# Optimization experiments

Hardware: AMD Instinct MI355X
Metric: run time of the kernel (lower is better)

## Reference

```python
import jax, jax.numpy as jnp
import numpy as np
import math

B, SQ, SK, DQ, DK, DV = 8, 1024, 1024, 512, 512, 512


def setup_inputs() -> dict:
    key = jax.random.key(0)
    ks = jax.random.split(key, 12)
    s = lambda fan_in: 1.0 / math.sqrt(fan_in)
    return {
        "Q": jax.random.normal(ks[0], (B, SQ, DQ), jnp.float32),
        "K": jax.random.normal(ks[1], (B, SK, DK), jnp.float32),
        "Wq": jax.random.uniform(ks[2], (DV, DQ), jnp.float32, -s(DQ), s(DQ)),
        "bq": jax.random.uniform(ks[3], (DV,), jnp.float32, -s(DQ), s(DQ)),
        "Wk": jax.random.uniform(ks[4], (DV, DK), jnp.float32, -s(DK), s(DK)),
        "bk": jax.random.uniform(ks[5], (DV,), jnp.float32, -s(DK), s(DK)),
        "Wv": jax.random.uniform(ks[6], (DV, DK), jnp.float32, -s(DK), s(DK)),
        "bv": jax.random.uniform(ks[7], (DV,), jnp.float32, -s(DK), s(DK)),
        "Wo": jax.random.uniform(ks[8], (DV, DV), jnp.float32, -s(DV), s(DV)),
        "bo": jax.random.uniform(ks[9], (DV,), jnp.float32, -s(DV), s(DV)),
        "num_heads": 8,
    }


def reference(Q, K, Wq, bq, Wk, bk, Wv, bv, Wo, bo, num_heads):
    dim_V = Wq.shape[0]
    dh = dim_V // num_heads
    b, sq, _ = Q.shape
    sk = K.shape[1]
    # projections (torch Linear: x @ W.T + b)
    Qp = Q @ Wq.T + bq                      # [B, Sq, Dv]
    Kp = K @ Wk.T + bk                      # [B, Sk, Dv]
    Vp = K @ Wv.T + bv                      # [B, Sk, Dv]
    # manual head split (split along feature, cat along batch) == reshape to heads
    Qh = Qp.reshape(b, sq, num_heads, dh)   # [B, Sq, H, dh]
    Kh = Kp.reshape(b, sk, num_heads, dh)
    Vh = Vp.reshape(b, sk, num_heads, dh)
    # NOTE: scale is sqrt(dim_V), not sqrt(head_dim), as in the source.
    scores = jnp.einsum("bqhd,bkhd->bhqk", Qh, Kh) / jnp.sqrt(
        jnp.asarray(dim_V, Qh.dtype))
    A = jax.nn.softmax(scores, axis=-1)     # [B, H, Sq, Sk]
    ctx = jnp.einsum("bhqk,bkhd->bqhd", A, Vh)
    O = (Qh + ctx).reshape(b, sq, dim_V)    # residual on projected Q, merge heads
    O = O + jax.nn.relu(O @ Wo.T + bo)      # FFN residual
    return O
```

## Files before the change

### kernel.cpp

```cpp
#include <hip/hip_runtime.h>

typedef unsigned short u16;
typedef __attribute__((ext_vector_type(8))) short short8;
typedef __attribute__((ext_vector_type(4))) float f32x4;
typedef __attribute__((ext_vector_type(2))) unsigned uint2v;

__device__ __forceinline__ u16 f2bf(float f) {
  union { float f; unsigned u; } v; v.f = f;
  unsigned r = v.u + 0x7FFFu + ((v.u >> 16) & 1u);
  return (u16)(r >> 16);
}
__device__ __forceinline__ float bf2f(u16 u) {
  union { unsigned u; float f; } v; v.u = ((unsigned)u) << 16;
  return v.f;
}
__device__ __forceinline__ void gload_lds16(const u16* g, u16* l) {
  __builtin_amdgcn_global_load_lds((const __attribute__((address_space(1))) void*)g,
                                   (__attribute__((address_space(3))) void*)l,
                                   16, 0, 0);
}

#if __has_builtin(__builtin_amdgcn_exp2f)
#define EXP2(x) __builtin_amdgcn_exp2f(x)
#else
#define EXP2(x) exp2f(x)
#endif

#define BATCH 8
#define SEQ   1024
#define DIM   512
#define NH    8
#define DH    64
#define MROWS (BATCH * SEQ)

__global__ void cvt_all(const float* __restrict__ Q, const float* __restrict__ K,
                        const float* __restrict__ Wq, const float* __restrict__ Wk,
                        const float* __restrict__ Wv, const float* __restrict__ Wo,
                        u16* __restrict__ Qbf, u16* __restrict__ Kbf,
                        u16* __restrict__ Wbf) {
  const int gb = blockIdx.x;
  const float4* src;
  u16* dst;
  int i;
  if (gb < 4096) {
    src = (const float4*)Q; dst = Qbf; i = gb * 256 + threadIdx.x;
  } else if (gb < 8192) {
    src = (const float4*)K; dst = Kbf; i = (gb - 4096) * 256 + threadIdx.x;
  } else {
    const int wb = gb - 8192;
    const int wsel = wb >> 8;
    const float* w = (wsel == 0) ? Wq : (wsel == 1) ? Wk : (wsel == 2) ? Wv : Wo;
    src = (const float4*)w;
    dst = Wbf + (size_t)wsel * (DIM * DIM);
    i = (wb & 255) * 256 + threadIdx.x;
  }
  float4 v = src[i];
  ushort4 r;
  r.x = f2bf(v.x); r.y = f2bf(v.y); r.z = f2bf(v.z); r.w = f2bf(v.w);
  *(ushort4*)&dst[i * 4] = r;
}

__device__ __forceinline__ void gemm_core(const u16* __restrict__ A,
                                          const u16* __restrict__ W,
                                          u16* ldsA, u16* ldsB,
                                          int tid, int m0, int n0,
                                          f32x4 acc[4][4]) {
  const int lane = tid & 63;
  const int wv = tid >> 6;
  const int wr = wv >> 1, wc = wv & 1;
  const int lr = lane & 15, lg = lane >> 4;
  const int wbase = tid & 192;

#define STAGE(buf, kt)                                                          \
  {                                                                             \
    _Pragma("unroll")                                                           \
    for (int i = 0; i < 2; ++i) {                                               \
      const int T = i * 256 + tid;                                              \
      const int row = T & 127, kc = T >> 7;                                     \
      const int koff = (kt) * 32 + kc * 8;                                      \
      gload_lds16(A + (size_t)(m0 + row) * DIM + koff,                          \
                  ldsA + (buf) * 4096 + (i * 256 + wbase) * 8);                 \
      gload_lds16(W + (size_t)(n0 + row) * DIM + koff,                          \
                  ldsB + (buf) * 4096 + (i * 256 + wbase) * 8);                 \
    }                                                                           \
  }

  STAGE(0, 0);
  __syncthreads();
  int cur = 0;
#pragma unroll 1
  for (int kt = 0; kt < 16; ++kt) {
    if (kt < 15) STAGE(cur ^ 1, kt + 1);
    short8 av[4], bw[4];
#pragma unroll
    for (int m = 0; m < 4; ++m)
      av[m] = *(const short8*)(ldsA + cur * 4096 + (lg * 128 + wr * 64 + m * 16 + lr) * 8);
#pragma unroll
    for (int n = 0; n < 4; ++n)
      bw[n] = *(const short8*)(ldsB + cur * 4096 + (lg * 128 + wc * 64 + n * 16 + lr) * 8);
#pragma unroll
    for (int m = 0; m < 4; ++m)
#pragma unroll
      for (int n = 0; n < 4; ++n)
        acc[m][n] = __builtin_amdgcn_mfma_f32_16x16x32_bf16(av[m], bw[n], acc[m][n], 0, 0, 0);
    __syncthreads();
    cur ^= 1;
  }
#undef STAGE
}

__global__ __launch_bounds__(256, 2) void proj_gemm(
    const u16* __restrict__ Qbf, const u16* __restrict__ Kbf,
    const u16* __restrict__ Wbf,
    const float* __restrict__ bq, const float* __restrict__ bk,
    const float* __restrict__ bv,
    u16* __restrict__ Qp, u16* __restrict__ Kp, u16* __restrict__ VpT) {
  __shared__ alignas(16) u16 ldsA[2 * 4096];
  __shared__ alignas(16) u16 ldsB[2 * 4096];

  const int tid = threadIdx.x;
  const int z = blockIdx.z;
  const int m0 = blockIdx.x * 128;
  const int n0 = blockIdx.y * 128;

  const u16* A = (z == 0) ? Qbf : Kbf;
  const u16* W = Wbf + (size_t)z * (DIM * DIM);
  const float* bias = (z == 0) ? bq : (z == 1) ? bk : bv;

  f32x4 acc[4][4] = {};
  gemm_core(A, W, ldsA, ldsB, tid, m0, n0, acc);

  const int lane = tid & 63;
  const int wv = tid >> 6;
  const int wr = wv >> 1, wc = wv & 1;
  const int lr = lane & 15, lg = lane >> 4;

  float bn[4];
#pragma unroll
  for (int n = 0; n < 4; ++n) bn[n] = bias[n0 + wc * 64 + n * 16 + lr];

  if (z < 2) {
    u16* outp = (z == 0) ? Qp : Kp;
#pragma unroll
    for (int m = 0; m < 4; ++m)
#pragma unroll
      for (int n = 0; n < 4; ++n)
#pragma unroll
        for (int r = 0; r < 4; ++r) {
          const int row = m0 + wr * 64 + m * 16 + lg * 4 + r;
          const int col = n0 + wc * 64 + n * 16 + lr;
          outp[(size_t)row * DIM + col] = f2bf(acc[m][n][r] + bn[n]);
        }
  } else {
#pragma unroll
    for (int m = 0; m < 4; ++m)
#pragma unroll
      for (int n = 0; n < 4; ++n) {
        const int grow = m0 + wr * 64 + m * 16 + lg * 4;
        const int b = grow >> 10;
        const int s = grow & 1023;
        const int col = n0 + wc * 64 + n * 16 + lr;
        ushort4 pk;
        pk.x = f2bf(acc[m][n][0] + bn[n]);
        pk.y = f2bf(acc[m][n][1] + bn[n]);
        pk.z = f2bf(acc[m][n][2] + bn[n]);
        pk.w = f2bf(acc[m][n][3] + bn[n]);
        *(ushort4*)&VpT[(size_t)b * (DIM * SEQ) + (size_t)col * SEQ + s] = pk;
      }
  }
}

__global__ __launch_bounds__(512, 4) void attn_kernel(
    const u16* __restrict__ Qp, const u16* __restrict__ Kp,
    const u16* __restrict__ VpT, u16* __restrict__ Opre) {
  __shared__ alignas(16) u16 klds[2][8192];
  __shared__ alignas(16) u16 vlds[2][8192];
  __shared__ alignas(16) u16 plds[8][64 * 16];

  const int tid = threadIdx.x;
  const int lane = tid & 63, wv = tid >> 6;
  const int lr = lane & 15, lg = lane >> 4;
  const int q0 = blockIdx.y * 128;
  const int b = blockIdx.x >> 3, h = blockIdx.x & 7;
  const size_t rowbase = (size_t)b * SEQ;
  const int hoff = h * DH;

  const float csc = 0.063762f;
  short8 aq[2];
#pragma unroll
  for (int t = 0; t < 2; ++t) {
    short8 raw = *(const short8*)(Qp + (rowbase + q0 + wv * 16 + lr) * DIM +
                                  hoff + t * 32 + lg * 8);
    short8 s;
#pragma unroll
    for (int j = 0; j < 8; ++j) s[j] = (short)f2bf(bf2f((u16)raw[j]) * csc);
    aq[t] = s;
  }

#define STAGEKV(buf, kt)                                                        \
  {                                                                             \
    const int ks0_ = (kt) * 128;                                                \
    _Pragma("unroll")                                                           \
    for (int i = 0; i < 2; ++i) {                                               \
      const int T = i * 512 + tid;                                              \
      const int krr = T & 127, kcc = T >> 7;                                    \
      gload_lds16(Kp + (rowbase + ks0_ + krr) * DIM + hoff + kcc * 8,           \
                  &klds[buf][(i * 512 + (tid & 448)) * 8]);                     \
      const int vrr = T & 63, vcc = T >> 6;                                     \
      gload_lds16(VpT + (size_t)b * (DIM * SEQ) + (size_t)(hoff + vrr) * SEQ +  \
                      ks0_ + vcc * 8,                                           \
                  &vlds[buf][(i * 512 + (tid & 448)) * 8]);                     \
    }                                                                           \
  }

  u16* pw = &plds[wv][0];
  unsigned pbase = (unsigned)(uintptr_t)(__attribute__((address_space(3))) u16*)pw;
  const unsigned ta00 = pbase + (unsigned)lg * 128u;
  const unsigned ta01 = ta00 + 128u;
  const unsigned ta10 = ta00 + 1024u;
  const unsigned ta11 = ta00 + 1152u;

  float l_r[4] = {0.f, 0.f, 0.f, 0.f};
  f32x4 o_acc[4] = {};

  STAGEKV(0, 0);
  __syncthreads();

  int cur = 0;
#pragma unroll 1
  for (int kt = 0; kt < 8; ++kt) {
    if (kt < 7) STAGEKV(cur ^ 1, kt + 1);

#pragma unroll
    for (int hh = 0; hh < 2; ++hh) {
      f32x4 sa[4] = {};
      __builtin_amdgcn_s_setprio(1);
#pragma unroll
      for (int t = 0; t < 2; ++t)
#pragma unroll
        for (int f = 0; f < 4; ++f) {
          short8 bk_ = *(const short8*)(
              &klds[cur][((lg + 4 * t) * 128 + hh * 64 + f * 16 + lr) * 8]);
          sa[f] = __builtin_amdgcn_mfma_f32_16x16x32_bf16(aq[t], bk_, sa[f], 0, 0, 0);
        }
      __builtin_amdgcn_s_setprio(0);

      short8 bvf[8];
#pragma unroll
      for (int n = 0; n < 4; ++n)
#pragma unroll
        for (int t = 0; t < 2; ++t)
          bvf[n * 2 + t] = *(const short8*)(
              &vlds[cur][((8 * hh + 4 * t + lg) * 64 + n * 16 + lr) * 8]);

#pragma unroll
      for (int f = 0; f < 4; ++f) {
        float p0 = EXP2(sa[f][0]);
        float p1 = EXP2(sa[f][1]);
        float p2 = EXP2(sa[f][2]);
        float p3 = EXP2(sa[f][3]);
        l_r[0] += p0; l_r[1] += p1; l_r[2] += p2; l_r[3] += p3;
        unsigned lo, hi;
        asm("v_cvt_pk_bf16_f32 %0, %1, %2" : "=v"(lo) : "v"(p0), "v"(p1));
        asm("v_cvt_pk_bf16_f32 %0, %1, %2" : "=v"(hi) : "v"(p2), "v"(p3));
        uint2v pk; pk.x = lo; pk.y = hi;
        *(uint2v*)&pw[(f * 16 + lr) * 16 + lg * 4] = pk;
      }

      asm volatile("s_waitcnt lgkmcnt(0)" ::: "memory");
      uint2v t00, t01, t10, t11;
      asm volatile("ds_read_b64_tr_b16 %0, %1" : "=v"(t00) : "v"(ta00));
      asm volatile("ds_read_b64_tr_b16 %0, %1" : "=v"(t01) : "v"(ta01));
      asm volatile("ds_read_b64_tr_b16 %0, %1" : "=v"(t10) : "v"(ta10));
      asm volatile("ds_read_b64_tr_b16 %0, %1" : "=v"(t11) : "v"(ta11));
      asm volatile("s_waitcnt lgkmcnt(0)" ::: "memory");
      __builtin_amdgcn_sched_barrier(0);

      short8 ap[2];
      {
        union { unsigned u[4]; short8 s; } u0, u1;
        u0.u[0] = t00.x; u0.u[1] = t00.y; u0.u[2] = t01.x; u0.u[3] = t01.y;
        u1.u[0] = t10.x; u1.u[1] = t10.y; u1.u[2] = t11.x; u1.u[3] = t11.y;
        ap[0] = u0.s; ap[1] = u1.s;
      }

      __builtin_amdgcn_s_setprio(1);
#pragma unroll
      for (int n = 0; n < 4; ++n)
#pragma unroll
        for (int t = 0; t < 2; ++t)
          o_acc[n] = __builtin_amdgcn_mfma_f32_16x16x32_bf16(ap[t], bvf[n * 2 + t], o_acc[n], 0, 0, 0);
      __builtin_amdgcn_s_setprio(0);
    }

    __syncthreads();
    cur ^= 1;
  }
#undef STAGEKV

  float inv[4];
#pragma unroll
  for (int r = 0; r < 4; ++r) {
    float v = l_r[r];
#pragma unroll
    for (int msk = 1; msk < 16; msk <<= 1) v += __shfl_xor(v, msk);
    inv[r] = 1.0f / v;
  }
#pragma unroll
  for (int n = 0; n < 4; ++n)
#pragma unroll
    for (int r = 0; r < 4; ++r) {
      const size_t row = rowbase + q0 + wv * 16 + lg * 4 + r;
      const int col = hoff + n * 16 + lr;
      const float ctx = o_acc[n][r] * inv[r];
      const float qv = bf2f(Qp[row * DIM + col]);
      Opre[row * DIM + col] = f2bf(qv + ctx);
    }
}

__global__ __launch_bounds__(256, 2) void ffn_gemm(
    const u16* __restrict__ Opre, const u16* __restrict__ Wo_bf,
    const float* __restrict__ bo, float* __restrict__ out) {
  __shared__ alignas(16) u16 ldsA[2 * 4096];
  __shared__ alignas(16) u16 ldsB[2 * 4096];

  const int tid = threadIdx.x;
  const int m0 = blockIdx.x * 128;
  const int n0 = blockIdx.y * 128;

  f32x4 acc[4][4] = {};
  gemm_core(Opre, Wo_bf, ldsA, ldsB, tid, m0, n0, acc);

  const int lane = tid & 63;
  const int wv = tid >> 6;
  const int wr = wv >> 1, wc = wv & 1;
  const int lr = lane & 15, lg = lane >> 4;

  float bn[4];
#pragma unroll
  for (int n = 0; n < 4; ++n) bn[n] = bo[n0 + wc * 64 + n * 16 + lr];

#pragma unroll
  for (int m = 0; m < 4; ++m)
#pragma unroll
    for (int n = 0; n < 4; ++n)
#pragma unroll
      for (int r = 0; r < 4; ++r) {
        const int row = m0 + wr * 64 + m * 16 + lg * 4 + r;
        const int col = n0 + wc * 64 + n * 16 + lr;
        const float v = acc[m][n][r] + bn[n];
        const float o = bf2f(Opre[(size_t)row * DIM + col]);
        out[(size_t)row * DIM + col] = o + fmaxf(v, 0.f);
      }
}

extern "C" void kernel_launch(void* const* d_in, const int* in_sizes, int n_in,
                              void* d_out, int out_size, void* d_ws, size_t ws_size,
                              hipStream_t stream) {
  const float* Q  = (const float*)d_in[0];
  const float* K  = (const float*)d_in[1];
  const float* Wq = (const float*)d_in[2];
  const float* bq = (const float*)d_in[3];
  const float* Wk = (const float*)d_in[4];
  const float* bk = (const float*)d_in[5];
  const float* Wv = (const float*)d_in[6];
  const float* bv = (const float*)d_in[7];
  const float* Wo = (const float*)d_in[8];
  const float* bo = (const float*)d_in[9];

  char* ws = (char*)d_ws;
  const size_t SZ = (size_t)MROWS * DIM * sizeof(u16);
  u16* Qbf  = (u16*)(ws + 0);
  u16* Kbf  = (u16*)(ws + SZ);
  u16* Wbf  = (u16*)(ws + 2 * SZ);
  u16* Qp   = (u16*)(ws + 2 * SZ + 4 * (size_t)(DIM * DIM) * sizeof(u16));
  u16* Kp   = (u16*)((char*)Qp + SZ);
  u16* VpT  = (u16*)((char*)Kp + SZ);
  u16* Opre = (u16*)(ws + 0);

  cvt_all<<<dim3(9216), 256, 0, stream>>>(Q, K, Wq, Wk, Wv, Wo, Qbf, Kbf, Wbf);
  proj_gemm<<<dim3(64, 4, 3), 256, 0, stream>>>(Qbf, Kbf, Wbf, bq, bk, bv, Qp, Kp, VpT);
  attn_kernel<<<dim3(64, 8), 512, 0, stream>>>(Qp, Kp, VpT, Opre);
  ffn_gemm<<<dim3(64, 4), 256, 0, stream>>>(Opre, Wbf + 3 * (DIM * DIM), bo, (float*)d_out);
}
```

Baseline: 98.53 us.

## Halve attention KV tile and compute softmax row sums with MFMA against ones

The attention kernel now stages 64-key K/V tiles instead of 128, which halves LDS use per block and doubles the number of loop iterations and __syncthreads barriers. The softmax denominator is no longer accumulated in fp32 with a cross-lane shuffle reduction at the end. Instead it comes from two extra MFMAs that multiply the bf16 P tile by a vector of ones. The smaller LDS footprint may allow more resident blocks, at the cost of more barriers, and the row sums now use bf16-rounded probabilities.

```diff
diff --git a/kernel.cpp b/kernel.cpp
--- a/kernel.cpp
+++ b/kernel.cpp
@@ -173,8 +173,8 @@
 __global__ __launch_bounds__(512, 4) void attn_kernel(
     const u16* __restrict__ Qp, const u16* __restrict__ Kp,
     const u16* __restrict__ VpT, u16* __restrict__ Opre) {
-  __shared__ alignas(16) u16 klds[2][8192];
-  __shared__ alignas(16) u16 vlds[2][8192];
+  __shared__ alignas(16) u16 klds[2][4096];
+  __shared__ alignas(16) u16 vlds[2][4096];
   __shared__ alignas(16) u16 plds[8][64 * 16];
 
   const int tid = threadIdx.x;
@@ -197,20 +197,19 @@
     aq[t] = s;
   }
 
+  short8 ones;
+#pragma unroll
+  for (int j = 0; j < 8; ++j) ones[j] = (short)0x3F80;
+
 #define STAGEKV(buf, kt)                                                        \
   {                                                                             \
-    const int ks0_ = (kt) * 128;                                                \
-    _Pragma("unroll")                                                           \
-    for (int i = 0; i < 2; ++i) {                                               \
-      const int T = i * 512 + tid;                                              \
-      const int krr = T & 127, kcc = T >> 7;                                    \
-      gload_lds16(Kp + (rowbase + ks0_ + krr) * DIM + hoff + kcc * 8,           \
-                  &klds[buf][(i * 512 + (tid & 448)) * 8]);                     \
-      const int vrr = T & 63, vcc = T >> 6;                                     \
-      gload_lds16(VpT + (size_t)b * (DIM * SEQ) + (size_t)(hoff + vrr) * SEQ +  \
-                      ks0_ + vcc * 8,                                           \
-                  &vlds[buf][(i * 512 + (tid & 448)) * 8]);                     \
-    }                                                                           \
+    const int ks0_ = (kt) * 64;                                                 \
+    const int rr = tid & 63, cc = tid >> 6;                                     \
+    gload_lds16(Kp + (rowbase + ks0_ + rr) * DIM + hoff + cc * 8,               \
+                &klds[buf][tid * 8]);                                           \
+    gload_lds16(VpT + (size_t)b * (DIM * SEQ) + (size_t)(hoff + rr) * SEQ +     \
+                    ks0_ + cc * 8,                                              \
+                &vlds[buf][tid * 8]);                                           \
   }
 
   u16* pw = &plds[wv][0];
@@ -220,7 +219,7 @@
   const unsigned ta10 = ta00 + 1024u;
   const unsigned ta11 = ta00 + 1152u;
 
-  float l_r[4] = {0.f, 0.f, 0.f, 0.f};
+  f32x4 l_acc = {};
   f32x4 o_acc[4] = {};
 
   STAGEKV(0, 0);
@@ -228,70 +227,66 @@
 
   int cur = 0;
 #pragma unroll 1
-  for (int kt = 0; kt < 8; ++kt) {
-    if (kt < 7) STAGEKV(cur ^ 1, kt + 1);
-
-#pragma unroll
-    for (int hh = 0; hh < 2; ++hh) {
-      f32x4 sa[4] = {};
-      __builtin_amdgcn_s_setprio(1);
+  for (int kt = 0; kt < 16; ++kt) {
+    if (kt < 15) STAGEKV(cur ^ 1, kt + 1);
+
+    f32x4 sa[4] = {};
+    __builtin_amdgcn_s_setprio(1);
+#pragma unroll
+    for (int t = 0; t < 2; ++t)
+#pragma unroll
+      for (int f = 0; f < 4; ++f) {
+        short8 bk_ = *(const short8*)(&klds[cur][((lg + 4 * t) * 64 + f * 16 + lr) * 8]);
+        sa[f] = __builtin_amdgcn_mfma_f32_16x16x32_bf16(aq[t], bk_, sa[f], 0, 0, 0);
+      }
+    __builtin_amdgcn_s_setprio(0);
+
+    short8 bvf[8];
+#pragma unroll
+    for (int n = 0; n < 4; ++n)
 #pragma unroll
       for (int t = 0; t < 2; ++t)
-#pragma unroll
-        for (int f = 0; f < 4; ++f) {
-          short8 bk_ = *(const short8*)(
-              &klds[cur][((lg + 4 * t) * 128 + hh * 64 + f * 16 + lr) * 8]);
-          sa[f] = __builtin_amdgcn_mfma_f32_16x16x32_bf16(aq[t], bk_, sa[f], 0, 0, 0);
-        }
-      __builtin_amdgcn_s_setprio(0);
-
-      short8 bvf[8];
-#pragma unroll
-      for (int n = 0; n < 4; ++n)
-#pragma unroll
-        for (int t = 0; t < 2; ++t)
-          bvf[n * 2 + t] = *(const short8*)(
-              &vlds[cur][((8 * hh + 4 * t + lg) * 64 + n * 16 + lr) * 8]);
-
-#pragma unroll
-      for (int f = 0; f < 4; ++f) {
-        float p0 = EXP2(sa[f][0]);
-        float p1 = EXP2(sa[f][1]);
-        float p2 = EXP2(sa[f][2]);
-        float p3 = EXP2(sa[f][3]);
-        l_r[0] += p0; l_r[1] += p1; l_r[2] += p2; l_r[3] += p3;
-        unsigned lo, hi;
-        asm("v_cvt_pk_bf16_f32 %0, %1, %2" : "=v"(lo) : "v"(p0), "v"(p1));
-        asm("v_cvt_pk_bf16_f32 %0, %1, %2" : "=v"(hi) : "v"(p2), "v"(p3));
-        uint2v pk; pk.x = lo; pk.y = hi;
-        *(uint2v*)&pw[(f * 16 + lr) * 16 + lg * 4] = pk;
-      }
-
-      asm volatile("s_waitcnt lgkmcnt(0)" ::: "memory");
-      uint2v t00, t01, t10, t11;
-      asm volatile("ds_read_b64_tr_b16 %0, %1" : "=v"(t00) : "v"(ta00));
-      asm volatile("ds_read_b64_tr_b16 %0, %1" : "=v"(t01) : "v"(ta01));
-      asm volatile("ds_read_b64_tr_b16 %0, %1" : "=v"(t10) : "v"(ta10));
-      asm volatile("ds_read_b64_tr_b16 %0, %1" : "=v"(t11) : "v"(ta11));
-      asm volatile("s_waitcnt lgkmcnt(0)" ::: "memory");
-      __builtin_amdgcn_sched_barrier(0);
-
-      short8 ap[2];
-      {
-        union { unsigned u[4]; short8 s; } u0, u1;
-        u0.u[0] = t00.x; u0.u[1] = t00.y; u0.u[2] = t01.x; u0.u[3] = t01.y;
-        u1.u[0] = t10.x; u1.u[1] = t10.y; u1.u[2] = t11.x; u1.u[3] = t11.y;
-        ap[0] = u0.s; ap[1] = u1.s;
-      }
-
-      __builtin_amdgcn_s_setprio(1);
-#pragma unroll
-      for (int n = 0; n < 4; ++n)
-#pragma unroll
-        for (int t = 0; t < 2; ++t)
-          o_acc[n] = __builtin_amdgcn_mfma_f32_16x16x32_bf16(ap[t], bvf[n * 2 + t], o_acc[n], 0, 0, 0);
-      __builtin_amdgcn_s_setprio(0);
+        bvf[n * 2 + t] = *(const short8*)(&vlds[cur][((lg + 4 * t) * 64 + n * 16 + lr) * 8]);
+
+#pragma unroll
+    for (int f = 0; f < 4; ++f) {
+      float p0 = EXP2(sa[f][0]);
+      float p1 = EXP2(sa[f][1]);
+      float p2 = EXP2(sa[f][2]);
+      float p3 = EXP2(sa[f][3]);
+      unsigned lo, hi;
+      asm("v_cvt_pk_bf16_f32 %0, %1, %2" : "=v"(lo) : "v"(p0), "v"(p1));
+      asm("v_cvt_pk_bf16_f32 %0, %1, %2" : "=v"(hi) : "v"(p2), "v"(p3));
+      uint2v pk; pk.x = lo; pk.y = hi;
+      *(uint2v*)&pw[(f * 16 + lr) * 16 + lg * 4] = pk;
     }
+
+    asm volatile("s_waitcnt lgkmcnt(0)" ::: "memory");
+    uint2v t00, t01, t10, t11;
+    asm volatile("ds_read_b64_tr_b16 %0, %1" : "=v"(t00) : "v"(ta00));
+    asm volatile("ds_read_b64_tr_b16 %0, %1" : "=v"(t01) : "v"(ta01));
+    asm volatile("ds_read_b64_tr_b16 %0, %1" : "=v"(t10) : "v"(ta10));
+    asm volatile("ds_read_b64_tr_b16 %0, %1" : "=v"(t11) : "v"(ta11));
+    asm volatile("s_waitcnt lgkmcnt(0)" ::: "memory");
+    __builtin_amdgcn_sched_barrier(0);
+
+    short8 ap[2];
+    {
+      union { unsigned u[4]; short8 s; } u0, u1;
+      u0.u[0] = t00.x; u0.u[1] = t00.y; u0.u[2] = t01.x; u0.u[3] = t01.y;
+      u1.u[0] = t10.x; u1.u[1] = t10.y; u1.u[2] = t11.x; u1.u[3] = t11.y;
+      ap[0] = u0.s; ap[1] = u1.s;
+    }
+
+    __builtin_amdgcn_s_setprio(1);
+#pragma unroll
+    for (int n = 0; n < 4; ++n)
+#pragma unroll
+      for (int t = 0; t < 2; ++t)
+        o_acc[n] = __builtin_amdgcn_mfma_f32_16x16x32_bf16(ap[t], bvf[n * 2 + t], o_acc[n], 0, 0, 0);
+    l_acc = __builtin_amdgcn_mfma_f32_16x16x32_bf16(ap[0], ones, l_acc, 0, 0, 0);
+    l_acc = __builtin_amdgcn_mfma_f32_16x16x32_bf16(ap[1], ones, l_acc, 0, 0, 0);
+    __builtin_amdgcn_s_setprio(0);
 
     __syncthreads();
     cur ^= 1;
@@ -300,12 +295,7 @@
 
   float inv[4];
 #pragma unroll
-  for (int r = 0; r < 4; ++r) {
-    float v = l_r[r];
-#pragma unroll
-    for (int msk = 1; msk < 16; msk <<= 1) v += __shfl_xor(v, msk);
-    inv[r] = 1.0f / v;
-  }
+  for (int r = 0; r < 4; ++r) inv[r] = 1.0f / l_acc[r];
 #pragma unroll
   for (int n = 0; n < 4; ++n)
 #pragma unroll
```

Result: faster. 95.27 us (-3.3%).
